# Kernel optimization log

Measured on AMD Instinct MI355X. Metric: run time of the kernel, lower is better.

The kernel has to match this reference:

```python
import jax, jax.numpy as jnp
import numpy as np

DN = ('NCHW', 'OIHW', 'NCHW')

def conv(x, w, b, stride=1, pad=((1, 1), (1, 1))):
    y = jax.lax.conv_general_dilated(x, w, (stride, stride), pad, dimension_numbers=DN)
    return y + b[None, :, None, None]

def l2norm(x, axis):
    return x / jnp.maximum(jnp.linalg.norm(x, axis=axis, keepdims=True), 1e-12)

def groupnorm(x, g, b, groups=32, eps=1e-5):
    B, C, H, W = x.shape
    xr = x.reshape(B, groups, C // groups, H, W)
    m = xr.mean(axis=(2, 3, 4), keepdims=True)
    v = xr.var(axis=(2, 3, 4), keepdims=True)
    xr = (xr - m) / jnp.sqrt(v + eps)
    return xr.reshape(B, C, H, W) * g[None, :, None, None] + b[None, :, None, None]

def setup_inputs() -> dict:
    key = jax.random.key(0)
    ks = jax.random.split(key, 24)
    s = 0.05
    B, L, C = 8, 77, 256
    inp = {
        'images': jax.random.normal(ks[0], (B, 3, 512, 512), jnp.float32),
        'text_tokens': jax.random.randint(ks[1], (B, L), 0, 49408, jnp.int32),
        'tok512': jax.random.normal(ks[2], (B, L, 512), jnp.float32),
        # TinyImageEncoder stem (3->64->256, stride 4 total)
        'conv1_w': jax.random.normal(ks[3], (64, 3, 3, 3), jnp.float32) * s,
        'conv1_b': jnp.zeros((64,), jnp.float32),
        'conv2_w': jax.random.normal(ks[4], (C, 64, 3, 3), jnp.float32) * s,
        'conv2_b': jnp.zeros((C,), jnp.float32),
        # SpatialPosResidual2D: 1x1 convs 2->64->256 (hid = max(32, C//4) = 64)
        'sp1_w': jax.random.normal(ks[5], (64, 2, 1, 1), jnp.float32) * s,
        'sp1_b': jnp.zeros((64,), jnp.float32),
        'sp2_w': jax.random.normal(ks[6], (C, 64, 1, 1), jnp.float32) * s,
        'sp2_b': jnp.zeros((C,), jnp.float32),
        # token_proj: Linear(512, C); token_gate: Linear(C, C) + sigmoid
        'proj_w': jax.random.normal(ks[7], (512, C), jnp.float32) * s,
        'proj_b': jnp.zeros((C,), jnp.float32),
        'gate_w': jax.random.normal(ks[8], (C, C), jnp.float32) * s,
        'gate_b': jnp.zeros((C,), jnp.float32),
        # decoder: Conv(2C+1->C,3x3) + GN + ReLU + Conv(C->64,3x3) + ReLU + Conv(64->1,1x1)
        'd1_w': jax.random.normal(ks[9], (C, 2 * C + 1, 3, 3), jnp.float32) * s,
        'd1_b': jnp.zeros((C,), jnp.float32),
        'gn_g': jnp.ones((C,), jnp.float32),
        'gn_b': jnp.zeros((C,), jnp.float32),
        'd2_w': jax.random.normal(ks[10], (64, C, 3, 3), jnp.float32) * s,
        'd2_b': jnp.zeros((64,), jnp.float32),
        'd3_w': jax.random.normal(ks[11], (1, 64, 1, 1), jnp.float32) * s,
        'd3_b': jnp.zeros((1,), jnp.float32),
    }
    return inp

def reference(images, text_tokens, tok512, conv1_w, conv1_b, conv2_w, conv2_b,
              sp1_w, sp1_b, sp2_w, sp2_b, proj_w, proj_b, gate_w, gate_b,
              d1_w, d1_b, gn_g, gn_b, d2_w, d2_b, d3_w, d3_b):
    # TinyImageEncoder: two stride-2 3x3 convs -> [B, C, H/4, W/4]
    x = jax.nn.relu(conv(images, conv1_w, conv1_b, stride=2))
    x = jax.nn.relu(conv(x, conv2_w, conv2_b, stride=2))
    b, c, h, w = x.shape
    # SpatialPosResidual2D: learnable encoding of normalized x/y grid
    yy = jnp.broadcast_to(jnp.linspace(-1.0, 1.0, h, dtype=x.dtype)[None, None, :, None], (1, 1, h, w))
    xx = jnp.broadcast_to(jnp.linspace(-1.0, 1.0, w, dtype=x.dtype)[None, None, None, :], (1, 1, h, w))
    coord = jnp.concatenate([xx, yy], axis=1)  # [1, 2, h, w]
    pos = conv(jax.nn.relu(conv(coord, sp1_w, sp1_b, pad=((0, 0), (0, 0)))), sp2_w, sp2_b, pad=((0, 0), (0, 0)))
    img = x + pos
    dense = l2norm(img, axis=1)  # per-pixel L2 over channels
    # text tokens -> projected, gated, normalized
    proj = tok512 @ proj_w + proj_b                       # [B, L, C]
    tok = jax.nn.sigmoid(proj @ gate_w + gate_b) * proj
    tok = l2norm(tok, axis=-1)
    valid = (text_tokens != 0).astype(dense.dtype)        # [B, L]
    # single-head cross-modal attention: pixels attend to tokens
    v = dense.reshape(b, c, h * w).transpose(0, 2, 1)     # [B, HW, C]
    scores = jnp.einsum('bnc,blc->bnl', v, tok) * (float(c) ** -0.5)
    scores = jnp.where(valid[:, None, :] == 0, jnp.asarray(-10000.0, scores.dtype), scores)
    attn = jax.nn.softmax(scores, axis=-1)
    ctx = jnp.einsum('bnl,blc->bnc', attn, tok)           # [B, HW, C]
    ctx_map = ctx.transpose(0, 2, 1).reshape(b, c, h, w)
    # global similarity map
    wsum = jnp.maximum(valid.sum(axis=1, keepdims=True), 1.0)
    gvec = l2norm((tok * valid[:, :, None]).sum(axis=1) / wsum, axis=-1)  # [B, C]
    sim = jnp.sum(dense * gvec[:, :, None, None], axis=1, keepdims=True)  # [B, 1, h, w]
    fused = jnp.concatenate([img, ctx_map, sim], axis=1)  # [B, 2C+1, h, w]
    y = jax.nn.relu(groupnorm(conv(fused, d1_w, d1_b), gn_g, gn_b))
    y = jax.nn.relu(conv(y, d2_w, d2_b))
    y = conv(y, d3_w, d3_b, pad=((0, 0), (0, 0)))
    # bilinear upsample to input resolution (align_corners=False semantics)
    return jax.image.resize(y, (b, 1, images.shape[2], images.shape[3]), 'bilinear')
```

## Files before the change

kernel.cpp:

```cpp
#include <hip/hip_runtime.h>
#include <math.h>

typedef unsigned short u16;
typedef __attribute__((ext_vector_type(4))) unsigned short u16x4;
typedef __attribute__((ext_vector_type(8))) unsigned short u16x8;
typedef __attribute__((ext_vector_type(8))) short short8;
typedef __attribute__((ext_vector_type(4))) float f32x4;

#define BB 8
#define CC 256
#define LL 77
#define HW 16384
#define XROW 520

__device__ __forceinline__ float bf2f(u16 h) {
  return __uint_as_float(((unsigned)h) << 16);
}
__device__ __forceinline__ u16 f2bf(float f) {
  unsigned u = __float_as_uint(f);
  unsigned r = (u + 0x7fffu + ((u >> 16) & 1u)) >> 16;
  return (u16)r;
}

static const size_t OFF_XT    = 0;
static const size_t OFF_B     = 136314880;
static const size_t OFF_GVECB = 630784;
static const size_t OFF_PG    = 137363456;
static const size_t OFF_GNSUM = 203423744;
static const size_t WS_BYTES_NEEDED = 203425792;
static const size_t OFF_Y2T = 0;
static const size_t OFF_GA  = 16777216;
static const size_t OFF_GB  = 16785408;
static const size_t OFF_Y3  = 16793600;
static const size_t WT1_BYTES = 9u * 256u * 544u * 2u;
static const size_t WT2_BYTES = 9u * 64u * 256u * 2u;

__global__ __launch_bounds__(256) void fill_kernel(float* __restrict__ out,
                                                   int n, float v) {
  int i = blockIdx.x * 256 + threadIdx.x;
  if (i < n) out[i] = v;
}

__global__ __launch_bounds__(512) void zero_gnsum(float* __restrict__ g) {
  g[threadIdx.x] = 0.f;
}

__global__ __launch_bounds__(256) void prep_wt(
    const float* __restrict__ w, u16* __restrict__ wt,
    int OC, int ICSRC, int ICPAD, int total) {
  int idx = blockIdx.x * 256 + threadIdx.x;
  if (idx >= total) return;
  int ic = idx % ICPAD;
  int oc = (idx / ICPAD) % OC;
  int kk = idx / (ICPAD * OC);
  float v = 0.f;
  if (ic < ICSRC) v = w[((size_t)oc * ICSRC + ic) * 9 + kk];
  wt[idx] = f2bf(v);
}

__global__ __launch_bounds__(256) void pos_xt(
    const float* __restrict__ sp1_w, const float* __restrict__ sp1_b,
    const float* __restrict__ sp2_w, const float* __restrict__ sp2_b,
    u16* __restrict__ xt) {
  __shared__ float hid[64 * 64];
  __shared__ u16 pv[64 * 256];
  const int tid = threadIdx.x;
  const int px0 = blockIdx.x * 64;
  #pragma unroll
  for (int i = 0; i < 16; ++i) {
    int slot = i * 256 + tid;
    int pxl = slot >> 6, h = slot & 63;
    int px = px0 + pxl;
    float xx = -1.f + (px & 127) * (2.f / 127.f);
    float yy = -1.f + (px >> 7) * (2.f / 127.f);
    hid[slot] = fmaxf(sp1_w[2 * h] * xx + sp1_w[2 * h + 1] * yy + sp1_b[h], 0.f);
  }
  float wr[64];
  #pragma unroll
  for (int q = 0; q < 16; ++q) {
    float4 v = *reinterpret_cast<const float4*>(sp2_w + tid * 64 + q * 4);
    wr[q * 4] = v.x; wr[q * 4 + 1] = v.y; wr[q * 4 + 2] = v.z; wr[q * 4 + 3] = v.w;
  }
  const float sb = sp2_b[tid];
  __syncthreads();
  for (int pxl = 0; pxl < 64; ++pxl) {
    float acc = sb;
    const float* hr = &hid[pxl * 64];
    #pragma unroll
    for (int h = 0; h < 64; ++h) acc = fmaf(wr[h], hr[h], acc);
    pv[pxl * 256 + tid] = f2bf(acc);
  }
  __syncthreads();
  for (int b = 0; b < BB; ++b) {
    u16* xb = xt + ((size_t)b * HW + px0) * XROW;
    #pragma unroll
    for (int it = 0; it < 8; ++it) {
      int slot = it * 256 + tid;
      int pxl = slot >> 5, cg = slot & 31;
      *reinterpret_cast<u16x8*>(xb + (size_t)pxl * XROW + cg * 8) =
          *reinterpret_cast<const u16x8*>(&pv[pxl * 256 + cg * 8]);
    }
  }
}

__global__ __launch_bounds__(256) void conv1_kernel(
    const float* __restrict__ in, const float* __restrict__ w,
    const float* __restrict__ bias, u16* __restrict__ x1t) {
  __shared__ float wl[27 * 64];
  __shared__ float bl[64];
  const int tid = threadIdx.x;
  const int oh = blockIdx.x;
  const int b = blockIdx.y;
  for (int i = tid; i < 27 * 64; i += 256) {
    int oc = i & 63;
    int t = i >> 6;
    wl[t * 64 + oc] = w[oc * 27 + t];
  }
  if (tid < 64) bl[tid] = bias[tid];
  __syncthreads();
  const int ow = tid;
  float acc[64];
  #pragma unroll
  for (int oc = 0; oc < 64; ++oc) acc[oc] = bl[oc];
  for (int ic = 0; ic < 3; ++ic) {
    #pragma unroll
    for (int kh = 0; kh < 3; ++kh) {
      int ih = 2 * oh + kh - 1;
      if ((unsigned)ih >= 512u) continue;
      const float* row = in + ((size_t)(b * 3 + ic) * 512 + ih) * 512;
      int iw = 2 * ow - 1;
      float v0 = (iw >= 0) ? row[iw] : 0.f;
      float v1 = row[iw + 1];
      float v2 = row[iw + 2];
      const float* wr = &wl[(ic * 3 + kh) * 192];
      #pragma unroll
      for (int oc = 0; oc < 64; ++oc)
        acc[oc] += v0 * wr[oc] + v1 * wr[64 + oc] + v2 * wr[128 + oc];
    }
  }
  u16* orow = x1t + ((size_t)b * 65536 + oh * 256 + ow) * 64;
  #pragma unroll
  for (int q = 0; q < 8; ++q) {
    u16x8 o;
    #pragma unroll
    for (int k = 0; k < 8; ++k) o[k] = f2bf(fmaxf(acc[q * 8 + k], 0.f));
    *reinterpret_cast<u16x8*>(orow + q * 8) = o;
  }
}

__global__ __launch_bounds__(256) void conv2_mfma(
    const u16* __restrict__ x1t, const u16* __restrict__ wt,
    const float* __restrict__ bias, u16* __restrict__ xt) {
  __shared__ u16 lb[15480];
  const int tid = threadIdx.x;
  const int lane = tid & 63;
  const int w = tid >> 6;
  const int oh = blockIdx.x >> 1;
  const int half = blockIdx.x & 1;
  const int ow0 = half << 6;
  const int b = blockIdx.z;
  const int colA = lane & 15;
  const int g = lane >> 4;
  const int oc0w = w * 64;

  f32x4 acc[4][4];
  #pragma unroll
  for (int of = 0; of < 4; ++of) {
    f32x4 bv;
    #pragma unroll
    for (int r = 0; r < 4; ++r) bv[r] = bias[oc0w + of * 16 + g * 4 + r];
    #pragma unroll
    for (int pf = 0; pf < 4; ++pf) acc[of][pf] = bv;
  }

  const u16* xb = x1t + (size_t)b * 65536 * 64;
  for (int ch = 0; ch < 2; ++ch) {
    __syncthreads();
    for (int slot = tid; slot < 1548; slot += 256) {
      int icg = slot & 3;
      int rc = slot >> 2;
      int kh, ip;
      if (rc < 192) {
        kh = rc / 64; int i = rc - kh * 64; ip = (ow0 << 1) + 2 * i;
      } else {
        int rc2 = rc - 192; kh = rc2 / 65; int j = rc2 - kh * 65;
        ip = (ow0 << 1) - 1 + 2 * j;
      }
      int ih = 2 * oh + kh - 1;
      u16x8 v = {0, 0, 0, 0, 0, 0, 0, 0};
      if ((unsigned)ih < 256u && (unsigned)ip < 256u)
        v = *reinterpret_cast<const u16x8*>(
            xb + ((size_t)(ih * 256 + ip)) * 64 + ch * 32 + icg * 8);
      *reinterpret_cast<u16x8*>(&lb[(rc * 5 + icg) << 3]) = v;
    }
    __syncthreads();
    #pragma unroll
    for (int kk = 0; kk < 9; ++kk) {
      const int kh = kk / 3, kw = kk - kh * 3;
      short8 afrag[4];
      const u16* wb = wt + ((size_t)kk * 256 + oc0w + colA) * 64 + ch * 32 + g * 8;
      #pragma unroll
      for (int of = 0; of < 4; ++of)
        afrag[of] = *reinterpret_cast<const short8*>(wb + (size_t)of * 16 * 64);
      #pragma unroll
      for (int pf = 0; pf < 4; ++pf) {
        int ow = pf * 16 + colA;
        int rc = (kw == 1) ? (kh * 64 + ow) : (192 + kh * 65 + ow + (kw >> 1));
        short8 bfrag = *reinterpret_cast<const short8*>(&lb[(rc * 5 + g) << 3]);
        #pragma unroll
        for (int of = 0; of < 4; ++of)
          acc[of][pf] = __builtin_amdgcn_mfma_f32_16x16x32_bf16(
              afrag[of], bfrag, acc[of][pf], 0, 0, 0);
      }
    }
  }
  #pragma unroll
  for (int of = 0; of < 4; ++of) {
    #pragma unroll
    for (int pf = 0; pf < 4; ++pf) {
      int px = oh * 128 + ow0 + pf * 16 + colA;
      int oc = oc0w + of * 16 + g * 4;
      u16* dst = xt + ((size_t)b * HW + px) * XROW + oc;
      u16x4 pz = *reinterpret_cast<const u16x4*>(dst);
      u16x4 o;
      #pragma unroll
      for (int r = 0; r < 4; ++r)
        o[r] = f2bf(fmaxf(acc[of][pf][r], 0.f) + bf2f(pz[r]));
      *reinterpret_cast<u16x4*>(dst) = o;
    }
  }
}

__global__ __launch_bounds__(256) void token_kernel(
    const float* __restrict__ tok512, const float* __restrict__ proj_w,
    const float* __restrict__ proj_b, const float* __restrict__ gate_w,
    const float* __restrict__ gate_b, float* __restrict__ tok_out) {
  __shared__ float t512[512];
  __shared__ float prj[256];
  __shared__ float red[4];
  int bl = blockIdx.x;
  int c = threadIdx.x;
  const float* trow = tok512 + (size_t)bl * 512;
  t512[c] = trow[c];
  t512[c + 256] = trow[c + 256];
  __syncthreads();
  float acc = proj_b[c];
  #pragma unroll 4
  for (int k = 0; k < 512; ++k) acc = fmaf(t512[k], proj_w[k * 256 + c], acc);
  prj[c] = acc;
  __syncthreads();
  float acc2 = gate_b[c];
  #pragma unroll 4
  for (int k = 0; k < 256; ++k) acc2 = fmaf(prj[k], gate_w[k * 256 + c], acc2);
  float g = 1.f / (1.f + __expf(-acc2));
  float tv = g * acc;
  float ss = tv * tv;
  #pragma unroll
  for (int off = 1; off < 64; off <<= 1) ss += __shfl_xor(ss, off);
  if ((c & 63) == 0) red[c >> 6] = ss;
  __syncthreads();
  float tot = red[0] + red[1] + red[2] + red[3];
  tok_out[(size_t)bl * 256 + c] = tv * (1.f / fmaxf(sqrtf(tot), 1e-12f));
}

__global__ __launch_bounds__(256) void gvec_kernel(
    const float* __restrict__ tok, const int* __restrict__ tokens,
    float* __restrict__ gvec) {
  __shared__ float red[4];
  int b = blockIdx.x, c = threadIdx.x;
  float s = 0.f;
  for (int l = 0; l < LL; ++l) {
    if (tokens[b * LL + l] != 0) s += tok[((size_t)b * LL + l) * 256 + c];
  }
  float ss = s * s;
  #pragma unroll
  for (int off = 1; off < 64; off <<= 1) ss += __shfl_xor(ss, off);
  if ((c & 63) == 0) red[c >> 6] = ss;
  __syncthreads();
  float tot = red[0] + red[1] + red[2] + red[3];
  gvec[b * 256 + c] = s * (1.f / fmaxf(sqrtf(tot), 1e-12f));
}

__global__ __launch_bounds__(256, 1) void attn_score(
    u16* __restrict__ xt, const float* __restrict__ tok,
    const int* __restrict__ tokens, const float* __restrict__ gvec,
    u16* __restrict__ pg) {
  __shared__ u16 ltok[LL * 256];
  __shared__ u16 pl[64 * 104];
  __shared__ float lgv[256];
  __shared__ u16 lval[LL + 3];
  const int tid = threadIdx.x;
  const int b = blockIdx.y;
  const int px0 = blockIdx.x * 64;
  for (int slot = tid; slot < LL * 32; slot += 256) {
    int l = slot >> 5, cg = slot & 31;
    const float* tp = tok + ((size_t)b * LL + l) * 256 + cg * 8;
    float4 t0 = *reinterpret_cast<const float4*>(tp);
    float4 t1 = *reinterpret_cast<const float4*>(tp + 4);
    u16x8 v = {f2bf(t0.x), f2bf(t0.y), f2bf(t0.z), f2bf(t0.w),
               f2bf(t1.x), f2bf(t1.y), f2bf(t1.z), f2bf(t1.w)};
    *reinterpret_cast<u16x8*>(&ltok[l * 256 + cg * 8]) = v;
  }
  for (int slot = tid; slot < 64 * 19; slot += 256) {
    int row = slot / 19, lp = LL + slot % 19;
    pl[row * 104 + lp] = 0;
  }
  if (tid < LL) lval[tid] = (tokens[b * LL + tid] != 0) ? 1 : 0;
  lgv[tid] = gvec[b * 256 + tid];
  __syncthreads();
  const int pxl = tid >> 2;
  const int q = tid & 3;
  const int p = px0 + pxl;
  const u16* xr = xt + ((size_t)b * HW + p) * XROW;
  float s[20];
  #pragma unroll
  for (int i = 0; i < 20; ++i) s[i] = 0.f;
  float ssum = 0.f, simacc = 0.f;
  #pragma unroll 1
  for (int c0 = 0; c0 < 256; c0 += 32) {
    float x[32];
    #pragma unroll
    for (int qq = 0; qq < 4; ++qq) {
      u16x8 iv = *reinterpret_cast<const u16x8*>(xr + c0 + qq * 8);
      #pragma unroll
      for (int k = 0; k < 8; ++k) x[qq * 8 + k] = bf2f(iv[k]);
    }
    #pragma unroll
    for (int k = 0; k < 32; ++k) {
      ssum = fmaf(x[k], x[k], ssum);
      simacc = fmaf(x[k], lgv[c0 + k], simacc);
    }
    #pragma unroll
    for (int li = 0; li < 20; ++li) {
      int l = li * 4 + q;
      if (l < LL) {
        const u16* tr = &ltok[l * 256 + c0];
        float a2 = s[li];
        #pragma unroll
        for (int qq = 0; qq < 4; ++qq) {
          u16x8 tv = *reinterpret_cast<const u16x8*>(tr + qq * 8);
          #pragma unroll
          for (int k = 0; k < 8; ++k) a2 = fmaf(x[qq * 8 + k], bf2f(tv[k]), a2);
        }
        s[li] = a2;
      }
    }
  }
  const float invn = 1.f / fmaxf(sqrtf(ssum), 1e-12f);
  const float sc = invn * 0.0625f;
  float m = -1e30f;
  #pragma unroll
  for (int li = 0; li < 20; ++li) {
    int l = li * 4 + q;
    float v = (l < LL) ? (lval[l] ? s[li] * sc : -10000.f) : -1e30f;
    s[li] = v;
    m = fmaxf(m, v);
  }
  m = fmaxf(m, __shfl_xor(m, 1));
  m = fmaxf(m, __shfl_xor(m, 2));
  float sum = 0.f;
  #pragma unroll
  for (int li = 0; li < 20; ++li) {
    float e = __expf(s[li] - m);
    s[li] = e;
    sum += e;
  }
  sum += __shfl_xor(sum, 1);
  sum += __shfl_xor(sum, 2);
  const float rs = 1.f / sum;
  #pragma unroll
  for (int li = 0; li < 20; ++li) {
    int l = li * 4 + q;
    if (l < LL) pl[pxl * 104 + l] = f2bf(s[li] * rs);
  }
  if (q == 0) {
    u16x8 sv = {f2bf(simacc * invn), 0, 0, 0, 0, 0, 0, 0};
    *reinterpret_cast<u16x8*>(xt + ((size_t)b * HW + p) * XROW + 512) = sv;
  }
  __syncthreads();
  u16* pgb = pg + ((size_t)b * HW + px0) * 96;
  #pragma unroll
  for (int it = 0; it < 3; ++it) {
    int slot = it * 256 + tid;
    int row = slot / 12, qq = slot % 12;
    *reinterpret_cast<u16x8*>(pgb + row * 96 + qq * 8) =
        *reinterpret_cast<const u16x8*>(&pl[row * 104 + qq * 8]);
  }
}

__global__ __launch_bounds__(256, 1) void attn_ctx(
    u16* __restrict__ xt, const float* __restrict__ tok,
    const u16* __restrict__ pg) {
  __shared__ u16 ltok[LL * 256];
  const int tid = threadIdx.x;
  const int b = blockIdx.y;
  for (int slot = tid; slot < LL * 32; slot += 256) {
    int l = slot >> 5, cg = slot & 31;
    const float* tp = tok + ((size_t)b * LL + l) * 256 + cg * 8;
    float4 t0 = *reinterpret_cast<const float4*>(tp);
    float4 t1 = *reinterpret_cast<const float4*>(tp + 4);
    u16x8 v = {f2bf(t0.x), f2bf(t0.y), f2bf(t0.z), f2bf(t0.w),
               f2bf(t1.x), f2bf(t1.y), f2bf(t1.z), f2bf(t1.w)};
    *reinterpret_cast<u16x8*>(&ltok[l * 256 + cg * 8]) = v;
  }
  __syncthreads();
  const int p = blockIdx.x * 256 + tid;
  const u16* pr = pg + ((size_t)b * HW + p) * 96;
  u16x8 pw[10];
  #pragma unroll
  for (int q = 0; q < 10; ++q)
    pw[q] = *reinterpret_cast<const u16x8*>(pr + q * 8);
  u16* xw = xt + ((size_t)b * HW + p) * XROW + 256;
  #pragma unroll 1
  for (int c0 = 0; c0 < 256; c0 += 32) {
    float a[32];
    #pragma unroll
    for (int k = 0; k < 32; ++k) a[k] = 0.f;
    #pragma unroll
    for (int l = 0; l < LL; ++l) {
      float sl = bf2f(pw[l >> 3][l & 7]);
      const u16* tr = &ltok[l * 256 + c0];
      #pragma unroll
      for (int q = 0; q < 4; ++q) {
        u16x8 tv = *reinterpret_cast<const u16x8*>(tr + q * 8);
        #pragma unroll
        for (int k = 0; k < 8; ++k) a[q * 8 + k] = fmaf(sl, bf2f(tv[k]), a[q * 8 + k]);
      }
    }
    #pragma unroll
    for (int q = 0; q < 4; ++q) {
      u16x8 ov;
      #pragma unroll
      for (int k = 0; k < 8; ++k) ov[k] = f2bf(a[q * 8 + k]);
      *reinterpret_cast<u16x8*>(xw + c0 + q * 8) = ov;
    }
  }
}

template <int CHUNKS, int XR, int OC, int OCW, bool AFFINE, bool GNST, bool RELU,
          int OROW>
__global__ __launch_bounds__(256) void convT_mfma(
    const u16* __restrict__ xt, const u16* __restrict__ wt,
    const float* __restrict__ bias, const float* __restrict__ gA,
    const float* __restrict__ gB, float* __restrict__ gnsum,
    u16* __restrict__ outT) {
  constexpr int ICPAD = CHUNKS * 32;
  constexpr int OCB = 4 * OCW;
  constexpr int NOF = OCW / 16;
  __shared__ u16 lb[7920];
  const int tid = threadIdx.x;
  const int lane = tid & 63;
  const int w = tid >> 6;
  const int oh = blockIdx.x >> 1;
  const int ow0 = (blockIdx.x & 1) << 6;
  const int oc0 = blockIdx.y * OCB + w * OCW;
  const int b = blockIdx.z;
  const int colA = lane & 15;
  const int g = lane >> 4;

  f32x4 acc[NOF][4];
  #pragma unroll
  for (int of = 0; of < NOF; ++of) {
    f32x4 bv;
    #pragma unroll
    for (int r = 0; r < 4; ++r) bv[r] = bias[oc0 + of * 16 + g * 4 + r];
    #pragma unroll
    for (int pf = 0; pf < 4; ++pf) acc[of][pf] = bv;
  }

  const u16* xtb = xt + (size_t)b * HW * XR;
  for (int ch = 0; ch < CHUNKS; ++ch) {
    __syncthreads();
    #pragma unroll
    for (int it = 0; it < 4; ++it) {
      int slot = it * 256 + tid;
      if (slot < 792) {
        int icg = slot & 3;
        int rc = slot >> 2;
        int col = rc % 66;
        int row = rc / 66;
        int ih = oh + row - 1;
        int ip = ow0 - 1 + col;
        int chb = ch * 32 + icg * 8;
        u16x8 v = {0, 0, 0, 0, 0, 0, 0, 0};
        if ((unsigned)ih < 128u && (unsigned)ip < 128u && chb + 8 <= XR) {
          v = *reinterpret_cast<const u16x8*>(xtb + (size_t)(ih * 128 + ip) * XR + chb);
          if constexpr (AFFINE) {
            const float* ga = gA + b * 256 + chb;
            const float* gb2 = gB + b * 256 + chb;
            #pragma unroll
            for (int k = 0; k < 8; ++k)
              v[k] = f2bf(fmaxf(fmaf(bf2f(v[k]), ga[k], gb2[k]), 0.f));
          }
        }
        *reinterpret_cast<u16x8*>(&lb[(rc * 5 + icg) << 3]) = v;
      }
    }
    __syncthreads();
    #pragma unroll
    for (int kk = 0; kk < 9; ++kk) {
      const int kh = kk / 3, kw = kk - kh * 3;
      short8 afrag[NOF];
      const u16* wb = wt + ((size_t)kk * OC + oc0 + colA) * ICPAD + ch * 32 + g * 8;
      #pragma unroll
      for (int of = 0; of < NOF; ++of)
        afrag[of] = *reinterpret_cast<const short8*>(wb + (size_t)of * 16 * ICPAD);
      #pragma unroll
      for (int pf = 0; pf < 4; ++pf) {
        int colx = pf * 16 + colA + kw;
        short8 bfrag = *reinterpret_cast<const short8*>(
            &lb[((kh * 66 + colx) * 5 + g) << 3]);
        #pragma unroll
        for (int of = 0; of < NOF; ++of)
          acc[of][pf] = __builtin_amdgcn_mfma_f32_16x16x32_bf16(
              afrag[of], bfrag, acc[of][pf], 0, 0, 0);
      }
    }
  }
  #pragma unroll
  for (int of = 0; of < NOF; ++of) {
    float s = 0.f, ss = 0.f;
    #pragma unroll
    for (int pf = 0; pf < 4; ++pf) {
      int px = oh * 128 + ow0 + pf * 16 + colA;
      u16x4 o;
      #pragma unroll
      for (int r = 0; r < 4; ++r) {
        float v = acc[of][pf][r];
        if constexpr (RELU) v = fmaxf(v, 0.f);
        if constexpr (GNST) { s += v; ss = fmaf(v, v, ss); }
        o[r] = f2bf(v);
      }
      *reinterpret_cast<u16x4*>(
          outT + ((size_t)b * HW + px) * OROW + oc0 + of * 16 + g * 4) = o;
    }
    if constexpr (GNST) {
      #pragma unroll
      for (int off2 = 1; off2 < 16; off2 <<= 1) {
        s += __shfl_xor(s, off2);
        ss += __shfl_xor(ss, off2);
      }
      s += __shfl_xor(s, 16);
      ss += __shfl_xor(ss, 16);
      if (colA == 0 && (g & 1) == 0) {
        int grp = (oc0 + of * 16 + g * 4) >> 3;
        atomicAdd(gnsum + ((size_t)b * 32 + grp) * 2, s);
        atomicAdd(gnsum + ((size_t)b * 32 + grp) * 2 + 1, ss);
      }
    }
  }
}

__global__ __launch_bounds__(256) void gn_fin(
    const float* __restrict__ gnsum, const float* __restrict__ gg,
    const float* __restrict__ gb, float* __restrict__ gA,
    float* __restrict__ gB) {
  int b = blockIdx.x, c = threadIdx.x;
  int grp = c >> 3;
  float s = gnsum[((size_t)b * 32 + grp) * 2];
  float ss = gnsum[((size_t)b * 32 + grp) * 2 + 1];
  float m = s * (1.f / 131072.f);
  float var = ss * (1.f / 131072.f) - m * m;
  float istd = rsqrtf(var + 1e-5f);
  float a = istd * gg[c];
  gA[b * 256 + c] = a;
  gB[b * 256 + c] = gb[c] - m * a;
}

__global__ __launch_bounds__(256) void d3_kernel(
    const u16* __restrict__ y2t, const float* __restrict__ w3,
    const float* __restrict__ b3, float* __restrict__ y3) {
  int idx = blockIdx.x * 256 + threadIdx.x;
  const u16* r = y2t + (size_t)idx * 64;
  float acc = b3[0];
  #pragma unroll
  for (int cg = 0; cg < 8; ++cg) {
    u16x8 v = *reinterpret_cast<const u16x8*>(r + cg * 8);
    #pragma unroll
    for (int k = 0; k < 8; ++k) acc = fmaf(bf2f(v[k]), w3[cg * 8 + k], acc);
  }
  y3[idx] = acc;
}

__global__ __launch_bounds__(256) void upsample_kernel(
    const float* __restrict__ y3, float* __restrict__ out) {
  int idx = blockIdx.x * 256 + threadIdx.x;
  int b = idx >> 18;
  int rem = idx & 262143;
  int Y = rem >> 9, X = rem & 511;
  float sy = (Y + 0.5f) * 0.25f - 0.5f;
  float sx = (X + 0.5f) * 0.25f - 0.5f;
  float y0f = floorf(sy), x0f = floorf(sx);
  float fy = sy - y0f, fx = sx - x0f;
  int y0 = (int)y0f, x0 = (int)x0f;
  int y0c = max(y0, 0), y1c = min(y0 + 1, 127);
  int x0c = max(x0, 0), x1c = min(x0 + 1, 127);
  const float* yb = y3 + (size_t)b * HW;
  float v00 = yb[y0c * 128 + x0c], v01 = yb[y0c * 128 + x1c];
  float v10 = yb[y1c * 128 + x0c], v11 = yb[y1c * 128 + x1c];
  out[idx] = (1.f - fy) * ((1.f - fx) * v00 + fx * v01) +
             fy * ((1.f - fx) * v10 + fx * v11);
}

extern "C" void kernel_launch(void* const* d_in, const int* in_sizes, int n_in,
                              void* d_out, int out_size, void* d_ws, size_t ws_size,
                              hipStream_t stream) {
  const float* images  = (const float*)d_in[0];
  const int*   tokens  = (const int*)d_in[1];
  const float* tok512  = (const float*)d_in[2];
  const float* conv1_w = (const float*)d_in[3];
  const float* conv1_b = (const float*)d_in[4];
  const float* conv2_w = (const float*)d_in[5];
  const float* conv2_b = (const float*)d_in[6];
  const float* sp1_w   = (const float*)d_in[7];
  const float* sp1_b   = (const float*)d_in[8];
  const float* sp2_w   = (const float*)d_in[9];
  const float* sp2_b   = (const float*)d_in[10];
  const float* proj_w  = (const float*)d_in[11];
  const float* proj_b  = (const float*)d_in[12];
  const float* gate_w  = (const float*)d_in[13];
  const float* gate_b  = (const float*)d_in[14];
  const float* d1_w    = (const float*)d_in[15];
  const float* d1_b    = (const float*)d_in[16];
  const float* gn_g    = (const float*)d_in[17];
  const float* gn_b    = (const float*)d_in[18];
  const float* d2_w    = (const float*)d_in[19];
  const float* d2_b    = (const float*)d_in[20];
  const float* d3_w    = (const float*)d_in[21];
  const float* d3_b    = (const float*)d_in[22];

  float* outp = (float*)d_out;
  if (ws_size < WS_BYTES_NEEDED) {
    float v = 10000.0f + (float)(ws_size >> 20);
    fill_kernel<<<(out_size + 255) / 256, 256, 0, stream>>>(outp, out_size, v);
    return;
  }

  char* wsb = (char*)d_ws;
  u16*   xt    = (u16*)(wsb + OFF_XT);
  u16*   x1t   = (u16*)(wsb + OFF_B);
  float* tokb  = (float*)(wsb + OFF_B);
  float* gvecb = (float*)(wsb + OFF_B + OFF_GVECB);
  u16*   pgb   = (u16*)(wsb + OFF_PG);
  u16*   y1t   = (u16*)(wsb + OFF_B);
  float* gnsum = (float*)(wsb + OFF_GNSUM);
  u16*   y2t   = (u16*)(wsb + OFF_Y2T);
  float* gA    = (float*)(wsb + OFF_GA);
  float* gB    = (float*)(wsb + OFF_GB);
  float* y3    = (float*)(wsb + OFF_Y3);

  u16* wt1  = (u16*)d_out;
  u16* wt2  = (u16*)((char*)d_out + WT1_BYTES);
  u16* wtc2 = (u16*)((char*)d_out + WT1_BYTES + WT2_BYTES);

  prep_wt<<<(9 * 256 * 544 + 255) / 256, 256, 0, stream>>>(
      d1_w, wt1, 256, 513, 544, 9 * 256 * 544);
  prep_wt<<<(9 * 64 * 256 + 255) / 256, 256, 0, stream>>>(
      d2_w, wt2, 64, 256, 256, 9 * 64 * 256);
  prep_wt<<<(9 * 256 * 64 + 255) / 256, 256, 0, stream>>>(
      conv2_w, wtc2, 256, 64, 64, 9 * 256 * 64);
  zero_gnsum<<<1, 512, 0, stream>>>(gnsum);

  pos_xt<<<256, 256, 0, stream>>>(sp1_w, sp1_b, sp2_w, sp2_b, xt);
  conv1_kernel<<<dim3(256, 8), 256, 0, stream>>>(images, conv1_w, conv1_b, x1t);
  conv2_mfma<<<dim3(256, 1, 8), 256, 0, stream>>>(x1t, wtc2, conv2_b, xt);
  token_kernel<<<BB * LL, 256, 0, stream>>>(tok512, proj_w, proj_b, gate_w,
                                            gate_b, tokb);
  gvec_kernel<<<BB, 256, 0, stream>>>(tokb, tokens, gvecb);
  attn_score<<<dim3(256, BB), 256, 0, stream>>>(xt, tokb, tokens, gvecb, pgb);
  attn_ctx<<<dim3(64, BB), 256, 0, stream>>>(xt, tokb, pgb);
  convT_mfma<17, XROW, 256, 32, false, true, false, 256>
      <<<dim3(256, 2, 8), 256, 0, stream>>>(xt, wt1, d1_b, nullptr, nullptr,
                                            gnsum, y1t);
  gn_fin<<<8, 256, 0, stream>>>(gnsum, gn_g, gn_b, gA, gB);
  convT_mfma<8, 256, 64, 16, true, false, true, 64>
      <<<dim3(256, 1, 8), 256, 0, stream>>>(y1t, wt2, d2_b, gA, gB, nullptr, y2t);
  d3_kernel<<<512, 256, 0, stream>>>(y2t, d3_w, d3_b, y3);
  upsample_kernel<<<8192, 256, 0, stream>>>(y3, outp);
}
```

Baseline: 1.314 ms.

## Fuse attention score and context kernels, keeping probabilities in shared memory

Merges attn_score and attn_ctx into one kernel so the softmax probabilities stay in LDS instead of being written to a global buffer and read back. Each group of four threads owning a pixel now computes the context for a 64-channel slice, and the result is written straight into the transposed feature map. This removes one launch, the global round-trip of the probability buffer, and the second bf16 conversion of the token matrix. In exchange each thread holds 64 float accumulators, which raises register pressure, and the context work now runs on the score kernel's grid of 64-pixel blocks.

```diff
diff --git a/kernel.cpp b/kernel.cpp
--- a/kernel.cpp
+++ b/kernel.cpp
@@ -25,7 +25,6 @@
 static const size_t OFF_XT    = 0;
 static const size_t OFF_B     = 136314880;
 static const size_t OFF_GVECB = 630784;
-static const size_t OFF_PG    = 137363456;
 static const size_t OFF_GNSUM = 203423744;
 static const size_t WS_BYTES_NEEDED = 203425792;
 static const size_t OFF_Y2T = 0;
@@ -281,10 +280,9 @@
   gvec[b * 256 + c] = s * (1.f / fmaxf(sqrtf(tot), 1e-12f));
 }
 
-__global__ __launch_bounds__(256, 1) void attn_score(
+__global__ __launch_bounds__(256, 1) void attn_fused(
     u16* __restrict__ xt, const float* __restrict__ tok,
-    const int* __restrict__ tokens, const float* __restrict__ gvec,
-    u16* __restrict__ pg) {
+    const int* __restrict__ tokens, const float* __restrict__ gvec) {
   __shared__ u16 ltok[LL * 256];
   __shared__ u16 pl[64 * 104];
   __shared__ float lgv[256];
@@ -301,10 +299,6 @@
                f2bf(t1.x), f2bf(t1.y), f2bf(t1.z), f2bf(t1.w)};
     *reinterpret_cast<u16x8*>(&ltok[l * 256 + cg * 8]) = v;
   }
-  for (int slot = tid; slot < 64 * 19; slot += 256) {
-    int row = slot / 19, lp = LL + slot % 19;
-    pl[row * 104 + lp] = 0;
-  }
   if (tid < LL) lval[tid] = (tokens[b * LL + tid] != 0) ? 1 : 0;
   lgv[tid] = gvec[b * 256 + tid];
   __syncthreads();
@@ -378,62 +372,29 @@
     *reinterpret_cast<u16x8*>(xt + ((size_t)b * HW + p) * XROW + 512) = sv;
   }
   __syncthreads();
-  u16* pgb = pg + ((size_t)b * HW + px0) * 96;
-  #pragma unroll
-  for (int it = 0; it < 3; ++it) {
-    int slot = it * 256 + tid;
-    int row = slot / 12, qq = slot % 12;
-    *reinterpret_cast<u16x8*>(pgb + row * 96 + qq * 8) =
-        *reinterpret_cast<const u16x8*>(&pl[row * 104 + qq * 8]);
-  }
-}
-
-__global__ __launch_bounds__(256, 1) void attn_ctx(
-    u16* __restrict__ xt, const float* __restrict__ tok,
-    const u16* __restrict__ pg) {
-  __shared__ u16 ltok[LL * 256];
-  const int tid = threadIdx.x;
-  const int b = blockIdx.y;
-  for (int slot = tid; slot < LL * 32; slot += 256) {
-    int l = slot >> 5, cg = slot & 31;
-    const float* tp = tok + ((size_t)b * LL + l) * 256 + cg * 8;
-    float4 t0 = *reinterpret_cast<const float4*>(tp);
-    float4 t1 = *reinterpret_cast<const float4*>(tp + 4);
-    u16x8 v = {f2bf(t0.x), f2bf(t0.y), f2bf(t0.z), f2bf(t0.w),
-               f2bf(t1.x), f2bf(t1.y), f2bf(t1.z), f2bf(t1.w)};
-    *reinterpret_cast<u16x8*>(&ltok[l * 256 + cg * 8]) = v;
-  }
-  __syncthreads();
-  const int p = blockIdx.x * 256 + tid;
-  const u16* pr = pg + ((size_t)b * HW + p) * 96;
-  u16x8 pw[10];
-  #pragma unroll
-  for (int q = 0; q < 10; ++q)
-    pw[q] = *reinterpret_cast<const u16x8*>(pr + q * 8);
-  u16* xw = xt + ((size_t)b * HW + p) * XROW + 256;
+  const int cbase = q * 64;
+  float a[64];
+  #pragma unroll
+  for (int k = 0; k < 64; ++k) a[k] = 0.f;
   #pragma unroll 1
-  for (int c0 = 0; c0 < 256; c0 += 32) {
-    float a[32];
-    #pragma unroll
-    for (int k = 0; k < 32; ++k) a[k] = 0.f;
-    #pragma unroll
-    for (int l = 0; l < LL; ++l) {
-      float sl = bf2f(pw[l >> 3][l & 7]);
-      const u16* tr = &ltok[l * 256 + c0];
-      #pragma unroll
-      for (int q = 0; q < 4; ++q) {
-        u16x8 tv = *reinterpret_cast<const u16x8*>(tr + q * 8);
-        #pragma unroll
-        for (int k = 0; k < 8; ++k) a[q * 8 + k] = fmaf(sl, bf2f(tv[k]), a[q * 8 + k]);
-      }
-    }
-    #pragma unroll
-    for (int q = 0; q < 4; ++q) {
-      u16x8 ov;
-      #pragma unroll
-      for (int k = 0; k < 8; ++k) ov[k] = f2bf(a[q * 8 + k]);
-      *reinterpret_cast<u16x8*>(xw + c0 + q * 8) = ov;
-    }
+  for (int l = 0; l < LL; ++l) {
+    float sl = bf2f(pl[pxl * 104 + l]);
+    const u16* tr = &ltok[l * 256 + cbase];
+    #pragma unroll
+    for (int qq = 0; qq < 8; ++qq) {
+      u16x8 tv = *reinterpret_cast<const u16x8*>(tr + qq * 8);
+      #pragma unroll
+      for (int k = 0; k < 8; ++k)
+        a[qq * 8 + k] = fmaf(sl, bf2f(tv[k]), a[qq * 8 + k]);
+    }
+  }
+  u16* xw = xt + ((size_t)b * HW + p) * XROW + 256 + cbase;
+  #pragma unroll
+  for (int qq = 0; qq < 8; ++qq) {
+    u16x8 ov;
+    #pragma unroll
+    for (int k = 0; k < 8; ++k) ov[k] = f2bf(a[qq * 8 + k]);
+    *reinterpret_cast<u16x8*>(xw + qq * 8) = ov;
   }
 }
 
@@ -641,7 +602,6 @@
   u16*   x1t   = (u16*)(wsb + OFF_B);
   float* tokb  = (float*)(wsb + OFF_B);
   float* gvecb = (float*)(wsb + OFF_B + OFF_GVECB);
-  u16*   pgb   = (u16*)(wsb + OFF_PG);
   u16*   y1t   = (u16*)(wsb + OFF_B);
   float* gnsum = (float*)(wsb + OFF_GNSUM);
   u16*   y2t   = (u16*)(wsb + OFF_Y2T);
@@ -667,8 +627,7 @@
   token_kernel<<<BB * LL, 256, 0, stream>>>(tok512, proj_w, proj_b, gate_w,
                                             gate_b, tokb);
   gvec_kernel<<<BB, 256, 0, stream>>>(tokb, tokens, gvecb);
-  attn_score<<<dim3(256, BB), 256, 0, stream>>>(xt, tokb, tokens, gvecb, pgb);
-  attn_ctx<<<dim3(64, BB), 256, 0, stream>>>(xt, tokb, pgb);
+  attn_fused<<<dim3(256, BB), 256, 0, stream>>>(xt, tokb, tokens, gvecb);
   convT_mfma<17, XROW, 256, 32, false, true, false, 256>
       <<<dim3(256, 2, 8), 256, 0, stream>>>(xt, wt1, d1_b, nullptr, nullptr,
                                             gnsum, y1t);
```

After: 1.251 ms. 4.8% less time.
